# Kernel optimization log

Hardware: AMD Instinct MI355X
Metric: run time of the kernel (lower is better)

The kernel has to match this reference:

```python
import jax, jax.numpy as jnp
import numpy as np

DIM_IN = 1024
DIM_Q = 1024
DIM_K = 1024
DIM_V = 1024
HEADS = 16

def setup_inputs() -> dict:
    key = jax.random.key(0)
    ks = jax.random.split(key, 5)
    s = 1.0 / np.sqrt(DIM_IN)
    return {
        "x": jax.random.normal(ks[0], (2, 2048, DIM_IN), dtype=jnp.float32),
        "Wq": jax.random.uniform(ks[1], (DIM_IN, DIM_Q), jnp.float32, -s, s),
        "Wk": jax.random.uniform(ks[2], (DIM_IN, DIM_K), jnp.float32, -s, s),
        "Wv": jax.random.uniform(ks[3], (DIM_IN, DIM_V), jnp.float32, -s, s),
        "Wo": jax.random.uniform(ks[4], (DIM_V, DIM_V), jnp.float32, -1.0/np.sqrt(DIM_V), 1.0/np.sqrt(DIM_V)),
    }

def reference(x, Wq, Wk, Wv, Wo):
    B, S, _ = x.shape
    H = HEADS
    q = (x @ Wq).reshape(B, S, H, DIM_Q // H).transpose(0, 2, 1, 3)  # [B,H,S,dq]
    k = (x @ Wk).reshape(B, S, H, DIM_K // H).transpose(0, 2, 1, 3)
    v = (x @ Wv).reshape(B, S, H, DIM_V // H).transpose(0, 2, 1, 3)
    scores = jnp.einsum("bhsd,bhtd->bhst", q, k)  # no pre-softmax scaling (as in source)
    # NOTE: source divides by sqrt(dim_q) AFTER softmax — replicated faithfully.
    attn = jax.nn.softmax(scores, axis=-1) / jnp.sqrt(jnp.float32(DIM_Q))
    out = jnp.einsum("bhst,bhtd->bhsd", attn, v)  # [B,H,S,dv]
    out = out.transpose(0, 2, 1, 3).reshape(B, S, DIM_V)
    return out @ Wo
```

## Files before the change

kernel.cpp:

```cpp
#include <hip/hip_runtime.h>
#include <hip/hip_bf16.h>


typedef __attribute__((ext_vector_type(8))) short bf16x8;
typedef __attribute__((ext_vector_type(4))) short short4v;
typedef __attribute__((ext_vector_type(4))) float f32x4;
typedef __attribute__((ext_vector_type(2))) unsigned int u32x2;

typedef const __attribute__((address_space(1))) void gvoid_t;
typedef __attribute__((address_space(3))) void svoid_t;
#define GLDS16(g, l) \
  __builtin_amdgcn_global_load_lds((gvoid_t*)(g), (svoid_t*)(l), 16, 0, 0)

#define MFMA16(a, b, c) __builtin_amdgcn_mfma_f32_16x16x32_bf16((a), (b), (c), 0, 0, 0)

#if defined(__has_builtin)
#if __has_builtin(__builtin_amdgcn_exp2f)
#define EXP2(x) __builtin_amdgcn_exp2f(x)
#else
#define EXP2(x) exp2f(x)
#endif
#else
#define EXP2(x) exp2f(x)
#endif

#define LOG2E 1.4426950408889634f
#define NSHIFT 17.312340490667561f

static __device__ __forceinline__ short f2bf(float f) {
  __hip_bfloat16 h = __float2bfloat16(f);
  short s;
  __builtin_memcpy(&s, &h, 2);
  return s;
}

static __device__ __forceinline__ unsigned pack2bf(float lo, float hi) {
  float2 t; t.x = lo; t.y = hi;
  __hip_bfloat162 h2 = __float22bfloat162_rn(t);
  unsigned u;
  __builtin_memcpy(&u, &h2, 4);
  return u;
}

__global__ __launch_bounds__(256) void prep(const float* __restrict__ x,
                                            const float* __restrict__ Wq,
                                            const float* __restrict__ Wk,
                                            const float* __restrict__ Wv,
                                            const float* __restrict__ Wo,
                                            short* __restrict__ xb,
                                            short* __restrict__ wqkvt,
                                            short* __restrict__ wot) {
  __shared__ float tile[64][65];
  int bid = blockIdx.x;
  int tid = threadIdx.x;
  if (bid < 2048) {
    int i = bid * 256 + tid;
    const float4* p = (const float4*)(x + (size_t)i * 8);
    float4 a = p[0], b = p[1];
    bf16x8 o;
    o[0] = f2bf(a.x); o[1] = f2bf(a.y); o[2] = f2bf(a.z); o[3] = f2bf(a.w);
    o[4] = f2bf(b.x); o[5] = f2bf(b.y); o[6] = f2bf(b.z); o[7] = f2bf(b.w);
    *(bf16x8*)(xb + (size_t)i * 8) = o;
    return;
  }
  bid -= 2048;
  int mat = bid >> 8;
  int t = bid & 255;
  int tn = (t & 15) * 64;
  int tk = (t >> 4) * 64;
  const float* src = (mat == 0) ? Wq : (mat == 1) ? Wk : (mat == 2) ? Wv : Wo;
  short* dst = (mat < 3) ? (wqkvt + (size_t)mat * 1024 * 1024) : wot;

  int c4 = (tid & 15) * 4;
#pragma unroll
  for (int it = 0; it < 4; ++it) {
    int r = (tid >> 4) + it * 16;
    float4 v = *(const float4*)(src + (size_t)(tk + r) * 1024 + tn + c4);
    tile[r][c4 + 0] = v.x; tile[r][c4 + 1] = v.y;
    tile[r][c4 + 2] = v.z; tile[r][c4 + 3] = v.w;
  }
  __syncthreads();
  int n = tid >> 2;
  int kc = (tid & 3) * 16;
  bf16x8 o0, o1;
#pragma unroll
  for (int j = 0; j < 8; ++j) {
    o0[j] = f2bf(tile[kc + j][n]);
    o1[j] = f2bf(tile[kc + 8 + j][n]);
  }
  *(bf16x8*)(dst + (size_t)(tn + n) * 1024 + tk + kc) = o0;
  *(bf16x8*)(dst + (size_t)(tn + n) * 1024 + tk + kc + 8) = o1;
}

__global__ __launch_bounds__(512, 4) void gemm_qkv(const short* __restrict__ A,
                                                   const short* __restrict__ Bt,
                                                   short* __restrict__ qk,
                                                   short* __restrict__ vt) {
  constexpr int K = 1024;
  __shared__ short As[2][128 * 64];
  __shared__ short Bs[2][192 * 64];
  const int tid = threadIdx.x;
  const int lane = tid & 63;
  const int w = tid >> 6;
  const int lr = lane & 15, lg = lane >> 4;
  const int m0 = blockIdx.y * 128, n0 = blockIdx.x * 192;
  const int wm = (w >> 2) * 64, wn = (w & 3) * 48;

  auto stage = [&](int kt, int bb) {
#pragma unroll
    for (int it = 0; it < 2; ++it) {
      int id = it * 512 + tid;
      int row = id >> 3, c = id & 7;
      int sc = c ^ (row & 7);
      GLDS16(A + (size_t)(m0 + row) * K + kt + sc * 8, &As[bb][0] + id * 8);
    }
#pragma unroll
    for (int it = 0; it < 3; ++it) {
      int id = it * 512 + tid;
      int row = id >> 3, c = id & 7;
      int sc = c ^ (row & 7);
      GLDS16(Bt + (size_t)(n0 + row) * K + kt + sc * 8, &Bs[bb][0] + id * 8);
    }
  };

  f32x4 acc[4][3] = {};

  stage(0, 0);
  __syncthreads();

  int cur = 0;
  for (int kt = 0; kt < K; kt += 64) {
    if (kt + 64 < K) stage(kt + 64, cur ^ 1);
    const short* Ab = &As[cur][0];
    const short* Bb = &Bs[cur][0];
#pragma unroll
    for (int kk2 = 0; kk2 < 2; ++kk2) {
      int cw = kk2 * 4 + lg;
      bf16x8 bfr[3];
#pragma unroll
      for (int ni = 0; ni < 3; ++ni) {
        int row = wn + ni * 16 + lr;
        bfr[ni] = *(const bf16x8*)(Bb + row * 64 + ((cw ^ (row & 7)) * 8));
      }
      __builtin_amdgcn_s_setprio(1);
#pragma unroll
      for (int mi = 0; mi < 4; ++mi) {
        int row = wm + mi * 16 + lr;
        bf16x8 af = *(const bf16x8*)(Ab + row * 64 + ((cw ^ (row & 7)) * 8));
#pragma unroll
        for (int ni = 0; ni < 3; ++ni)
          acc[mi][ni] = MFMA16(af, bfr[ni], acc[mi][ni]);
      }
      __builtin_amdgcn_s_setprio(0);
    }
    __syncthreads();
    cur ^= 1;
  }

#pragma unroll
  for (int mi = 0; mi < 4; ++mi) {
#pragma unroll
    for (int ni = 0; ni < 3; ++ni) {
      int m = m0 + wm + mi * 16 + lg * 4;
      int n = n0 + wn + ni * 16 + lr;
      if (n < 2048) {
        float sc = (n < 1024) ? LOG2E : 1.0f;
#pragma unroll
        for (int r = 0; r < 4; ++r)
          qk[(size_t)(m + r) * 2048 + n] = f2bf(acc[mi][ni][r] * sc);
      } else {
        int nv = n - 2048;
        int vtrow = ((m >> 11) * 16 + (nv >> 6)) * 64 + (nv & 63);
        int scol = m & 2047;
        int psc = (scol & ~31) | ((scol & 0xC) << 1) | ((scol & 16) >> 2) |
                  (scol & 3);
        short4v pv;
#pragma unroll
        for (int r = 0; r < 4; ++r) pv[r] = f2bf(acc[mi][ni][r]);
        *(short4v*)(vt + (size_t)vtrow * 2048 + psc) = pv;
      }
    }
  }
}

__global__ __launch_bounds__(256) void gemm_out(const short* __restrict__ A,
                                                const short* __restrict__ Bt,
                                                float* __restrict__ C) {
  constexpr int K = 1024, N = 1024;
  __shared__ short As[2][128 * 64];
  __shared__ short Bs[2][64 * 64];
  const int tid = threadIdx.x;
  const int lane = tid & 63;
  const int w = tid >> 6;
  const int lr = lane & 15, lg = lane >> 4;
  const int m0 = blockIdx.y * 128, n0 = blockIdx.x * 64;
  const int wm = (w >> 1) * 64, wn = (w & 1) * 32;

  auto stage = [&](int kt, int bb) {
#pragma unroll
    for (int it = 0; it < 4; ++it) {
      int id = it * 256 + tid;
      int row = id >> 3, c = id & 7;
      int sc = c ^ (row & 7);
      GLDS16(A + (size_t)(m0 + row) * K + kt + sc * 8, &As[bb][0] + id * 8);
    }
#pragma unroll
    for (int it = 0; it < 2; ++it) {
      int id = it * 256 + tid;
      int row = id >> 3, c = id & 7;
      int sc = c ^ (row & 7);
      GLDS16(Bt + (size_t)(n0 + row) * K + kt + sc * 8, &Bs[bb][0] + id * 8);
    }
  };

  f32x4 acc[4][2] = {};

  stage(0, 0);
  __syncthreads();

  int cur = 0;
  for (int kt = 0; kt < K; kt += 64) {
    if (kt + 64 < K) stage(kt + 64, cur ^ 1);
    const short* Ab = &As[cur][0];
    const short* Bb = &Bs[cur][0];
#pragma unroll
    for (int kk2 = 0; kk2 < 2; ++kk2) {
      int cw = kk2 * 4 + lg;
      bf16x8 bfr[2];
#pragma unroll
      for (int ni = 0; ni < 2; ++ni) {
        int row = wn + ni * 16 + lr;
        bfr[ni] = *(const bf16x8*)(Bb + row * 64 + ((cw ^ (row & 7)) * 8));
      }
      __builtin_amdgcn_s_setprio(1);
#pragma unroll
      for (int mi = 0; mi < 4; ++mi) {
        int row = wm + mi * 16 + lr;
        bf16x8 af = *(const bf16x8*)(Ab + row * 64 + ((cw ^ (row & 7)) * 8));
#pragma unroll
        for (int ni = 0; ni < 2; ++ni)
          acc[mi][ni] = MFMA16(af, bfr[ni], acc[mi][ni]);
      }
      __builtin_amdgcn_s_setprio(0);
    }
    __syncthreads();
    cur ^= 1;
  }

#pragma unroll
  for (int mi = 0; mi < 4; ++mi) {
#pragma unroll
    for (int ni = 0; ni < 2; ++ni) {
      int m = m0 + wm + mi * 16 + lg * 4;
      int n = n0 + wn + ni * 16 + lr;
#pragma unroll
      for (int r = 0; r < 4; ++r) C[(size_t)(m + r) * N + n] = acc[mi][ni][r];
    }
  }
}

__global__ __launch_bounds__(256, 2) void attn_fwd(const short* __restrict__ qk,
                                                   const short* __restrict__ vt,
                                                   short* __restrict__ outb) {
  constexpr int S = 2048, LDQ = 2048;
  const int fid = blockIdx.x;
  const int xcd = fid & 7, j = fid >> 3;
  const int qt = j & 15;
  const int pair = xcd * 4 + (j >> 4);
  const int h = pair & 15, b = pair >> 4;

  const int tid = threadIdx.x, lane = tid & 63, w = tid >> 6;
  const int lr = lane & 15, lg = lane >> 4;
  const int s7 = lr & 7;
  const int qb = qt * 128 + w * 32;

  __shared__ short Ks[2][128][64];
  __shared__ short Vs[2][64][128];

  const short* base = qk + (size_t)b * S * LDQ + h * 64;
  const short* vbase = vt + (size_t)(b * 16 + h) * 64 * 2048;

  bf16x8 qA0 = *(const bf16x8*)(base + (size_t)(qb + lr) * LDQ + lg * 8);
  bf16x8 qA1 = *(const bf16x8*)(base + (size_t)(qb + lr) * LDQ + 32 + lg * 8);
  bf16x8 qB0 = *(const bf16x8*)(base + (size_t)(qb + 16 + lr) * LDQ + lg * 8);
  bf16x8 qB1 = *(const bf16x8*)(base + (size_t)(qb + 16 + lr) * LDQ + 32 + lg * 8);

  bf16x8 ones;
#pragma unroll
  for (int i = 0; i < 8; ++i) ones[i] = (short)0x3F80;

  auto stage = [&](int kt, int bb) {
#pragma unroll
    for (int it = 0; it < 4; ++it) {
      int id = it * 256 + tid;
      {
        int row = id >> 3, c = id & 7;
        int sc = c ^ (row & 7);
        GLDS16(base + 1024 + (size_t)(kt + row) * LDQ + sc * 8,
               &Ks[bb][0][0] + id * 8);
      }
      {
        int row = id >> 4, c = id & 15;
        int sc = c ^ (row & 15);
        GLDS16(vbase + (size_t)row * 2048 + kt + sc * 8,
               &Vs[bb][0][0] + id * 8);
      }
    }
  };

  f32x4 oA[4] = {}, oB[4] = {};
  f32x4 laccA = {}, laccB = {};

  stage(0, 0);
  __syncthreads();

  int cur = 0;
  for (int kt = 0; kt < S; kt += 128) {
    if (kt + 128 < S) stage(kt + 128, cur ^ 1);

    const short* Kb = &Ks[cur][0][0];
    const short* Vb = &Vs[cur][0][0];

    f32x4 sA[8], sB[8];
    __builtin_amdgcn_s_setprio(1);
#pragma unroll
    for (int kc = 0; kc < 8; ++kc) {
      int krow = kc * 16 + lr;
      bf16x8 kf0 = *(const bf16x8*)(Kb + krow * 64 + ((lg ^ s7) * 8));
      bf16x8 kf1 = *(const bf16x8*)(Kb + krow * 64 + (((4 + lg) ^ s7) * 8));
      f32x4 s = {-NSHIFT, -NSHIFT, -NSHIFT, -NSHIFT};
      s = MFMA16(kf0, qA0, s);
      s = MFMA16(kf1, qA1, s);
      sA[kc] = s;
      f32x4 t = {-NSHIFT, -NSHIFT, -NSHIFT, -NSHIFT};
      t = MFMA16(kf0, qB0, t);
      t = MFMA16(kf1, qB1, t);
      sB[kc] = t;
    }
    __builtin_amdgcn_s_setprio(0);

    unsigned pwA[4][4], pwB[4][4];
#pragma unroll
    for (int kc = 0; kc < 8; ++kc) {
      {
        float p0 = EXP2(sA[kc][0]), p1 = EXP2(sA[kc][1]);
        float p2 = EXP2(sA[kc][2]), p3 = EXP2(sA[kc][3]);
        pwA[kc >> 1][(kc & 1) * 2 + 0] = pack2bf(p0, p1);
        pwA[kc >> 1][(kc & 1) * 2 + 1] = pack2bf(p2, p3);
      }
      {
        float p0 = EXP2(sB[kc][0]), p1 = EXP2(sB[kc][1]);
        float p2 = EXP2(sB[kc][2]), p3 = EXP2(sB[kc][3]);
        pwB[kc >> 1][(kc & 1) * 2 + 0] = pack2bf(p0, p1);
        pwB[kc >> 1][(kc & 1) * 2 + 1] = pack2bf(p2, p3);
      }
    }

    bf16x8 pA[4], pB[4];
#pragma unroll
    for (int g = 0; g < 4; ++g) {
      __builtin_memcpy(&pA[g], pwA[g], 16);
      __builtin_memcpy(&pB[g], pwB[g], 16);
    }

    __builtin_amdgcn_s_setprio(1);
#pragma unroll
    for (int g = 0; g < 4; ++g) {
      laccA = MFMA16(pA[g], ones, laccA);
      laccB = MFMA16(pB[g], ones, laccB);
    }
#pragma unroll
    for (int nc = 0; nc < 4; ++nc) {
      const short* vb = Vb + (nc * 16 + lr) * 128;
#pragma unroll
      for (int g = 0; g < 4; ++g) {
        bf16x8 vf = *(const bf16x8*)(vb + (((4 * g + lg) ^ lr) * 8));
        oA[nc] = MFMA16(pA[g], vf, oA[nc]);
        oB[nc] = MFMA16(pB[g], vf, oB[nc]);
      }
    }
    __builtin_amdgcn_s_setprio(0);
    __syncthreads();
    cur ^= 1;
  }

#pragma unroll
  for (int r = 0; r < 4; ++r) {
    float dA = 1.0f / (laccA[r] * 32.0f);
    float dB = 1.0f / (laccB[r] * 32.0f);
#pragma unroll
    for (int nc = 0; nc < 4; ++nc) {
      int col = h * 64 + nc * 16 + lr;
      outb[(size_t)(b * S + qb + 4 * lg + r) * 1024 + col] = f2bf(oA[nc][r] * dA);
      outb[(size_t)(b * S + qb + 16 + 4 * lg + r) * 1024 + col] =
          f2bf(oB[nc][r] * dB);
    }
  }
}

extern "C" void kernel_launch(void* const* d_in, const int* in_sizes, int n_in,
                              void* d_out, int out_size, void* d_ws,
                              size_t ws_size, hipStream_t stream) {
  (void)in_sizes; (void)n_in; (void)out_size; (void)ws_size;
  const float* x = (const float*)d_in[0];
  const float* Wq = (const float*)d_in[1];
  const float* Wk = (const float*)d_in[2];
  const float* Wv = (const float*)d_in[3];
  const float* Wo = (const float*)d_in[4];

  char* p = (char*)d_ws;
  short* xb = (short*)p;      p += (size_t)4096 * 1024 * 2;
  short* wqkvt = (short*)p;   p += (size_t)3072 * 1024 * 2;
  short* wot = (short*)p;     p += (size_t)1024 * 1024 * 2;
  short* qk = (short*)p;      p += (size_t)4096 * 2048 * 2;
  short* vt = (short*)p;      p += (size_t)4096 * 1024 * 2;
  short* attno = (short*)p;   p += (size_t)4096 * 1024 * 2;

  prep<<<3072, 256, 0, stream>>>(x, Wq, Wk, Wv, Wo, xb, wqkvt, wot);
  gemm_qkv<<<dim3(16, 32), 512, 0, stream>>>(xb, wqkvt, qk, vt);
  attn_fwd<<<512, 256, 0, stream>>>(qk, vt, attno);
  gemm_out<<<dim3(16, 32), 256, 0, stream>>>(attno, wot, (float*)d_out);
}
```

Measured before the change: 106.1 us.

## Software-pipeline attention loop so PV of previous tile overlaps current QK

The attention loop is restructured so the P·V and row-sum MFMAs for tile t-1 are issued after the QK^T MFMAs for tile t, and before the exp/pack of tile t. K and V staging are split: K is prefetched one tile ahead and V is loaded one tile behind. A tail block handles the final tile's P·V. The aim is to interleave VALU exp work with MFMA work and hide LDS/global latency. In exchange, P fragments stay live across iterations, which raises register pressure and could hurt occupancy at 2 waves/SIMD.

```diff
diff --git a/kernel.cpp b/kernel.cpp
--- a/kernel.cpp
+++ b/kernel.cpp
@@ -5,7 +5,6 @@
 typedef __attribute__((ext_vector_type(8))) short bf16x8;
 typedef __attribute__((ext_vector_type(4))) short short4v;
 typedef __attribute__((ext_vector_type(4))) float f32x4;
-typedef __attribute__((ext_vector_type(2))) unsigned int u32x2;
 
 typedef const __attribute__((address_space(1))) void gvoid_t;
 typedef __attribute__((address_space(3))) void svoid_t;
@@ -263,6 +262,7 @@
                                                    const short* __restrict__ vt,
                                                    short* __restrict__ outb) {
   constexpr int S = 2048, LDQ = 2048;
+  constexpr int NT = S / 128;
   const int fid = blockIdx.x;
   const int xcd = fid & 7, j = fid >> 3;
   const int qt = j & 15;
@@ -289,37 +289,40 @@
 #pragma unroll
   for (int i = 0; i < 8; ++i) ones[i] = (short)0x3F80;
 
-  auto stage = [&](int kt, int bb) {
+  auto stageK = [&](int kt, int bb) {
 #pragma unroll
     for (int it = 0; it < 4; ++it) {
       int id = it * 256 + tid;
-      {
-        int row = id >> 3, c = id & 7;
-        int sc = c ^ (row & 7);
-        GLDS16(base + 1024 + (size_t)(kt + row) * LDQ + sc * 8,
-               &Ks[bb][0][0] + id * 8);
-      }
-      {
-        int row = id >> 4, c = id & 15;
-        int sc = c ^ (row & 15);
-        GLDS16(vbase + (size_t)row * 2048 + kt + sc * 8,
-               &Vs[bb][0][0] + id * 8);
-      }
+      int row = id >> 3, c = id & 7;
+      int sc = c ^ (row & 7);
+      GLDS16(base + 1024 + (size_t)(kt + row) * LDQ + sc * 8,
+             &Ks[bb][0][0] + id * 8);
+    }
+  };
+  auto stageV = [&](int kt, int bb) {
+#pragma unroll
+    for (int it = 0; it < 4; ++it) {
+      int id = it * 256 + tid;
+      int row = id >> 4, c = id & 15;
+      int sc = c ^ (row & 15);
+      GLDS16(vbase + (size_t)row * 2048 + kt + sc * 8,
+             &Vs[bb][0][0] + id * 8);
     }
   };
 
   f32x4 oA[4] = {}, oB[4] = {};
   f32x4 laccA = {}, laccB = {};
-
-  stage(0, 0);
+  bf16x8 pA[4], pB[4];
+
+  stageK(0, 0);
   __syncthreads();
 
-  int cur = 0;
-  for (int kt = 0; kt < S; kt += 128) {
-    if (kt + 128 < S) stage(kt + 128, cur ^ 1);
-
-    const short* Kb = &Ks[cur][0][0];
-    const short* Vb = &Vs[cur][0][0];
+  for (int t = 0; t < NT; ++t) {
+    const int cb = t & 1;
+    if (t + 1 < NT) stageK((t + 1) * 128, cb ^ 1);
+    stageV(t * 128, cb);
+
+    const short* Kb = &Ks[cb][0][0];
 
     f32x4 sA[8], sB[8];
     __builtin_amdgcn_s_setprio(1);
@@ -332,12 +335,33 @@
       s = MFMA16(kf0, qA0, s);
       s = MFMA16(kf1, qA1, s);
       sA[kc] = s;
-      f32x4 t = {-NSHIFT, -NSHIFT, -NSHIFT, -NSHIFT};
-      t = MFMA16(kf0, qB0, t);
-      t = MFMA16(kf1, qB1, t);
-      sB[kc] = t;
+      f32x4 u = {-NSHIFT, -NSHIFT, -NSHIFT, -NSHIFT};
+      u = MFMA16(kf0, qB0, u);
+      u = MFMA16(kf1, qB1, u);
+      sB[kc] = u;
     }
     __builtin_amdgcn_s_setprio(0);
+
+    if (t > 0) {
+      const short* Vb = &Vs[cb ^ 1][0][0];
+      __builtin_amdgcn_s_setprio(1);
+#pragma unroll
+      for (int g = 0; g < 4; ++g) {
+        laccA = MFMA16(pA[g], ones, laccA);
+        laccB = MFMA16(pB[g], ones, laccB);
+      }
+#pragma unroll
+      for (int nc = 0; nc < 4; ++nc) {
+        const short* vb = Vb + (nc * 16 + lr) * 128;
+#pragma unroll
+        for (int g = 0; g < 4; ++g) {
+          bf16x8 vf = *(const bf16x8*)(vb + (((4 * g + lg) ^ lr) * 8));
+          oA[nc] = MFMA16(pA[g], vf, oA[nc]);
+          oB[nc] = MFMA16(pB[g], vf, oB[nc]);
+        }
+      }
+      __builtin_amdgcn_s_setprio(0);
+    }
 
     unsigned pwA[4][4], pwB[4][4];
 #pragma unroll
@@ -355,15 +379,17 @@
         pwB[kc >> 1][(kc & 1) * 2 + 1] = pack2bf(p2, p3);
       }
     }
-
-    bf16x8 pA[4], pB[4];
 #pragma unroll
     for (int g = 0; g < 4; ++g) {
       __builtin_memcpy(&pA[g], pwA[g], 16);
       __builtin_memcpy(&pB[g], pwB[g], 16);
     }
 
-    __builtin_amdgcn_s_setprio(1);
+    __syncthreads();
+  }
+
+  {
+    const short* Vb = &Vs[(NT - 1) & 1][0][0];
 #pragma unroll
     for (int g = 0; g < 4; ++g) {
       laccA = MFMA16(pA[g], ones, laccA);
@@ -379,9 +405,6 @@
         oB[nc] = MFMA16(pB[g], vf, oB[nc]);
       }
     }
-    __builtin_amdgcn_s_setprio(0);
-    __syncthreads();
-    cur ^= 1;
   }
 
 #pragma unroll
```

Measured after the change: 102.8 us. 3.1% less time.
